# Kernel optimization log

Hardware: AMD Instinct MI355X
Metric: run time of the kernel (lower is better)

## Reference

```python
import jax, jax.numpy as jnp
import numpy as np

B, N, A = 8, 16384, 7
NUM_GROUP = 1024   # npoint / G
GROUP_SIZE = 32    # knn k / M


def setup_inputs() -> dict:
    key = jax.random.key(0)
    xyz = jax.random.uniform(key, (B, N, A), dtype=jnp.float32)
    return {"xyz": xyz}


def _farthest_point_sample(xyz, npoint):
    # xyz: [B, N, A]; distances computed on first 3 dims only.
    b, n, a = xyz.shape
    coords = xyz[:, :, :3]
    batch = jnp.arange(b)
    # Deterministic start index (original uses randint; any start is a valid FPS seed).
    init = (jnp.full((b, n), 1e10, dtype=xyz.dtype), jnp.zeros((b,), dtype=jnp.int32))

    def step(carry, _):
        distance, farthest = carry
        centroid = xyz[batch, farthest]                      # [B, A]
        d = jnp.sum((coords - centroid[:, None, :3]) ** 2, -1)  # [B, N]
        distance = jnp.minimum(distance, d)                  # masked update == min
        new_farthest = jnp.argmax(distance, axis=-1).astype(jnp.int32)
        return (distance, new_farthest), (farthest, centroid)

    _, (idxs, cents) = jax.lax.scan(step, init, None, length=npoint)
    centroids = jnp.swapaxes(idxs, 0, 1)        # [B, npoint]
    centroids_attrs = jnp.swapaxes(cents, 0, 1)  # [B, npoint, A]
    return centroids, centroids_attrs


def _knn(center, xyz, k):
    # Euclidean cdist over ALL A attributes (as in the original torch.cdist call).
    # Squared distance preserves topk ordering.
    c2 = jnp.sum(center ** 2, -1)[:, :, None]    # [B, G, 1]
    x2 = jnp.sum(xyz ** 2, -1)[:, None, :]       # [B, 1, N]
    d2 = c2 + x2 - 2.0 * jnp.einsum('bga,bna->bgn', center, xyz)  # [B, G, N]
    _, idx = jax.lax.top_k(-d2, k)               # smallest-k, ascending distance
    return idx


def reference(xyz):
    center_idx, centroids_attrs = _farthest_point_sample(xyz, NUM_GROUP)
    centroids_coors = centroids_attrs[:, :, :3]
    idx = _knn(centroids_attrs, xyz, GROUP_SIZE)             # [B, G, M]
    b = xyz.shape[0]
    neighborhood = xyz[jnp.arange(b)[:, None, None], idx]    # [B, G, M, A]
    neighborhood = jnp.concatenate(
        [neighborhood[..., :3] - centroids_coors[:, :, None, :],
         neighborhood[..., 3:]], axis=-1)
    return neighborhood, center_idx, centroids_attrs, centroids_coors
```

## Files before the change

### kernel.cpp

```cpp
#include <hip/hip_runtime.h>

#define N_PTS  16384
#define B_SZ   8
#define NGROUP 1024
#define KNN_K  32
#define ATTR   7

#define OFF_NB     0
#define OFF_IDX    (B_SZ * NGROUP * KNN_K * ATTR)
#define OFF_CATTR  (OFF_IDX + B_SZ * NGROUP)
#define OFF_CCOORD (OFF_CATTR + B_SZ * NGROUP * ATTR)

typedef float v2f __attribute__((ext_vector_type(2)));
typedef float f2u __attribute__((ext_vector_type(2), aligned(4)));

template <int CTRL>
__device__ __forceinline__ float fmax_dpp_step(float x) {
    int d = __builtin_amdgcn_update_dpp(__float_as_int(x), __float_as_int(x),
                                        CTRL, 0xf, 0xf, false);
    return fmaxf(x, __int_as_float(d));
}
template <int CTRL>
__device__ __forceinline__ unsigned umin_dpp_step(unsigned x) {
    unsigned d = (unsigned)__builtin_amdgcn_update_dpp((int)x, (int)x,
                                                       CTRL, 0xf, 0xf, false);
    return x < d ? x : d;
}

__device__ __forceinline__ float wave_max_f32(float x) {
    x = fmax_dpp_step<0x111>(x);
    x = fmax_dpp_step<0x112>(x);
    x = fmax_dpp_step<0x114>(x);
    x = fmax_dpp_step<0x118>(x);
    x = fmax_dpp_step<0x142>(x);
    x = fmax_dpp_step<0x143>(x);
    return __int_as_float(__builtin_amdgcn_readlane(__float_as_int(x), 63));
}
__device__ __forceinline__ unsigned wave_min_u32(unsigned x) {
    x = umin_dpp_step<0x111>(x);
    x = umin_dpp_step<0x112>(x);
    x = umin_dpp_step<0x114>(x);
    x = umin_dpp_step<0x118>(x);
    x = umin_dpp_step<0x142>(x);
    x = umin_dpp_step<0x143>(x);
    return (unsigned)__builtin_amdgcn_readlane((int)x, 63);
}

__global__ void prep_kernel(const float* __restrict__ xyz, float* __restrict__ x2,
                            float* __restrict__ xt) {
#pragma clang fp contract(off)
    int i = blockIdx.x * blockDim.x + threadIdx.x;
    if (i >= B_SZ * N_PTS) return;
    const int b = i >> 14;
    const int p = i & (N_PTS - 1);
    const float* q = xyz + (size_t)i * ATTR;
    f2u a01 = *(const f2u*)q;
    f2u a23 = *(const f2u*)(q + 2);
    f2u a45 = *(const f2u*)(q + 4);
    float a6 = q[6];
    float s = a01.x * a01.x;
    s = s + a01.y * a01.y;
    s = s + a23.x * a23.x;
    s = s + a23.y * a23.y;
    s = s + a45.x * a45.x;
    s = s + a45.y * a45.y;
    s = s + a6 * a6;
    x2[i] = s;
    float* T = xt + (size_t)b * ATTR * N_PTS + p;
    T[0 * N_PTS] = a01.x;
    T[1 * N_PTS] = a01.y;
    T[2 * N_PTS] = a23.x;
    T[3 * N_PTS] = a23.y;
    T[4 * N_PTS] = a45.x;
    T[5 * N_PTS] = a45.y;
    T[6 * N_PTS] = a6;
}

#define FOR16(M) M(0) M(1) M(2) M(3) M(4) M(5) M(6) M(7) \
                 M(8) M(9) M(10) M(11) M(12) M(13) M(14) M(15)

#define PT_DECL(J) v2f px##J, py##J, pz##J, pd##J;

#define PT_LOAD(J) { \
    const int p0 = t + ((2 * J) << 9); \
    const float* q0 = X + (size_t)p0 * ATTR; \
    const float* q1 = q0 + (size_t)512 * ATTR; \
    f2u u0 = *(const volatile f2u*)q0; float z0 = ((const volatile float*)q0)[2]; \
    f2u u1 = *(const volatile f2u*)q1; float z1 = ((const volatile float*)q1)[2]; \
    px##J = (v2f){u0.x, u1.x}; \
    py##J = (v2f){u0.y, u1.y}; \
    pz##J = (v2f){z0, z1}; \
    pd##J = (v2f){1e10f, 1e10f}; }

#define PT_STEP(J) { \
    v2f dx = px##J - cx2; \
    v2f dy = py##J - cy2; \
    v2f dz = pz##J - cz2; \
    v2f a  = dx * dx; \
    a = a + dy * dy; \
    a = a + dz * dz; \
    v2f nd; \
    nd.x = fminf(pd##J.x, a.x); \
    nd.y = fminf(pd##J.y, a.y); \
    pd##J = nd; \
    if (nd.x > best) { best = nd.x; bidx = t + ((2 * J) << 9); } \
    if (nd.y > best) { best = nd.y; bidx = t + ((2 * J + 1) << 9); } }

__global__ __launch_bounds__(512)
__attribute__((amdgpu_waves_per_eu(2, 2)))
void fps_kernel(const float* __restrict__ xyz, float* __restrict__ out) {
#pragma clang fp contract(off)
    const int b = blockIdx.x;
    const int t = threadIdx.x;
    const int lane = t & 63;
    const int w = t >> 6;
    const float* X = xyz + (size_t)b * N_PTS * ATTR;

    FOR16(PT_DECL)
    FOR16(PT_LOAD)

    __shared__ unsigned long long sbuf[2][8];
    __shared__ int sel[NGROUP];
    if (t == 0) sel[0] = 0;
    float cx = X[0], cy = X[1], cz = X[2];
    __syncthreads();

    for (int s = 0; s < NGROUP - 1; ++s) {
        const int par = s & 1;
        const v2f cx2 = {cx, cx}, cy2 = {cy, cy}, cz2 = {cz, cz};
        float best = -1.0f;
        int   bidx = 0;
        FOR16(PT_STEP)
        const float wm = wave_max_f32(best);
        const unsigned cand = (best == wm) ? (unsigned)bidx : 0xFFFFFFFFu;
        const unsigned widx = wave_min_u32(cand);
        if (lane == 0) {
            sbuf[par][w] = ((unsigned long long)__float_as_uint(wm) << 32) |
                           (unsigned)(N_PTS - widx);
        }
        __syncthreads();
        unsigned long long bk = sbuf[par][0];
#pragma unroll
        for (int i = 1; i < 8; ++i) {
            const unsigned long long k = sbuf[par][i];
            if (k > bk) bk = k;
        }
        const int win = N_PTS - (int)(unsigned)bk;
        const int sbidx = __builtin_amdgcn_readfirstlane(win);
        if (t == 0) sel[s + 1] = sbidx;
        const float* q = X + (size_t)sbidx * ATTR;
        cx = q[0]; cy = q[1]; cz = q[2];
    }
    __syncthreads();

    for (int g = t; g < NGROUP; g += 512) {
        const int idx = sel[g];
        const float* q = X + (size_t)idx * ATTR;
        float a0 = q[0], a1 = q[1], a2 = q[2], a3 = q[3], a4 = q[4], a5 = q[5], a6 = q[6];
        out[OFF_IDX + b * NGROUP + g] = (float)idx;
        float* ca = out + OFF_CATTR + (size_t)(b * NGROUP + g) * ATTR;
        ca[0] = a0; ca[1] = a1; ca[2] = a2; ca[3] = a3; ca[4] = a4; ca[5] = a5; ca[6] = a6;
        float* cc = out + OFF_CCOORD + (size_t)(b * NGROUP + g) * 3;
        cc[0] = a0; cc[1] = a1; cc[2] = a2;
    }
}

__device__ __forceinline__ void topk_insert(float d2, int p, int lane,
                                            float& ld, int& li, float& kd, int& ki) {
    const bool cand = (d2 < kd) || (d2 == kd && p < ki);
    unsigned long long mask = __ballot(cand);
    while (mask) {
        const int l = __ffsll(mask) - 1;
        mask &= mask - 1;
        const float dc = __shfl(d2, l);
        const int   pc = __shfl(p, l);
        if ((dc < kd) || (dc == kd && pc < ki)) {
            const bool before = (ld < dc) || (ld == dc && li < pc);
            const int pos = (int)__popcll(__ballot(before));
            const float sd = __shfl_up(ld, 1);
            const int   si = __shfl_up(li, 1);
            if (lane == pos)      { ld = dc; li = pc; }
            else if (lane > pos)  { ld = sd; li = si; }
            if (lane >= KNN_K)    { ld = __builtin_inff(); li = 0x7fffffff; }
            kd = __shfl(ld, KNN_K - 1);
            ki = __shfl(li, KNN_K - 1);
        }
    }
}

__global__ __launch_bounds__(256) void knn_kernel(const float* __restrict__ xyz,
                                                  const float* __restrict__ x2,
                                                  const float* __restrict__ xt,
                                                  float* __restrict__ out) {
#pragma clang fp contract(off)
    const int lane = threadIdx.x & 63;
    const int gg = blockIdx.x * 4 + (threadIdx.x >> 6);
    const int b  = gg >> 10;
    const float* X = xyz + (size_t)b * N_PTS * ATTR;

    const float* C = out + OFF_CATTR + (size_t)gg * ATTR;
    const float c0 = C[0], c1 = C[1], c2a = C[2], c3 = C[3], c4 = C[4], c5 = C[5], c6 = C[6];
    float csq = c0 * c0;
    csq = csq + c1 * c1;
    csq = csq + c2a * c2a;
    csq = csq + c3 * c3;
    csq = csq + c4 * c4;
    csq = csq + c5 * c5;
    csq = csq + c6 * c6;

    float ld = __builtin_inff();
    int   li = 0x7fffffff;
    float kd = __builtin_inff();
    int   ki = 0x7fffffff;

    if (xt != nullptr) {
        const float* T0 = xt + (size_t)b * ATTR * N_PTS;
        const float* T1 = T0 + N_PTS;
        const float* T2 = T1 + N_PTS;
        const float* T3 = T2 + N_PTS;
        const float* T4 = T3 + N_PTS;
        const float* T5 = T4 + N_PTS;
        const float* T6 = T5 + N_PTS;
        const float* XB = x2 + (size_t)b * N_PTS;
        for (int p0 = 0; p0 < N_PTS; p0 += 64) {
            const int p = p0 + lane;
            const float q0 = T0[p], q1 = T1[p], q2 = T2[p], q3 = T3[p];
            const float q4 = T4[p], q5 = T5[p], q6 = T6[p];
            float dot = c0 * q0;
            dot = dot + c1 * q1;
            dot = dot + c2a * q2;
            dot = dot + c3 * q3;
            dot = dot + c4 * q4;
            dot = dot + c5 * q5;
            dot = dot + c6 * q6;
            const float xx = XB[p];
            const float d2 = (csq + xx) - 2.0f * dot;
            topk_insert(d2, p, lane, ld, li, kd, ki);
        }
    } else {
        for (int p0 = 0; p0 < N_PTS; p0 += 64) {
            const int p = p0 + lane;
            const float* q = X + (size_t)p * ATTR;
            float dot = c0 * q[0];
            dot = dot + c1 * q[1];
            dot = dot + c2a * q[2];
            dot = dot + c3 * q[3];
            dot = dot + c4 * q[4];
            dot = dot + c5 * q[5];
            dot = dot + c6 * q[6];
            float xx = q[0] * q[0];
            xx = xx + q[1] * q[1];
            xx = xx + q[2] * q[2];
            xx = xx + q[3] * q[3];
            xx = xx + q[4] * q[4];
            xx = xx + q[5] * q[5];
            xx = xx + q[6] * q[6];
            const float d2 = (csq + xx) - 2.0f * dot;
            topk_insert(d2, p, lane, ld, li, kd, ki);
        }
    }

    if (lane < KNN_K) {
        const float* q = X + (size_t)li * ATTR;
        float* o = out + OFF_NB + ((size_t)gg * KNN_K + lane) * ATTR;
        o[0] = q[0] - c0;
        o[1] = q[1] - c1;
        o[2] = q[2] - c2a;
        o[3] = q[3];
        o[4] = q[4];
        o[5] = q[5];
        o[6] = q[6];
    }
}

extern "C" void kernel_launch(void* const* d_in, const int* in_sizes, int n_in,
                              void* d_out, int out_size, void* d_ws, size_t ws_size,
                              hipStream_t stream) {
    const float* xyz = (const float*)d_in[0];
    float* out = (float*)d_out;

    const size_t need = (size_t)(B_SZ * N_PTS) * (1 + ATTR) * sizeof(float);
    const bool use_ws = ws_size >= need;
    float* x2 = use_ws ? (float*)d_ws : nullptr;
    float* xt = use_ws ? ((float*)d_ws + B_SZ * N_PTS) : nullptr;

    if (use_ws) {
        prep_kernel<<<(B_SZ * N_PTS + 255) / 256, 256, 0, stream>>>(xyz, x2, xt);
    }
    fps_kernel<<<B_SZ, 512, 0, stream>>>(xyz, out);
    knn_kernel<<<(B_SZ * NGROUP) / 4, 256, 0, stream>>>(xyz, x2, xt, out);
}
```

Measured before the change: 1.911 ms.

## Move FPS x/y point coordinates from registers to LDS, keep z and distances in VGPRs

The FPS kernel previously held x, y, z and the running min-distance for 32 points per thread in registers. It now stages x and y into shared memory (128 KB of LDS) and rereads them from LDS on every iteration, keeping only z and the distance in registers. An empty asm barrier pins the z values in VGPRs. Point assignment also changes to adjacent point pairs per thread, which gives contiguous loads. The intent is to relieve register pressure and spilling under the 512-thread launch bound, at the cost of 32 LDS reads per thread per FPS step.

```diff
diff --git a/kernel.cpp b/kernel.cpp
--- a/kernel.cpp
+++ b/kernel.cpp
@@ -79,22 +79,23 @@
 #define FOR16(M) M(0) M(1) M(2) M(3) M(4) M(5) M(6) M(7) \
                  M(8) M(9) M(10) M(11) M(12) M(13) M(14) M(15)
 
-#define PT_DECL(J) v2f px##J, py##J, pz##J, pd##J;
-
-#define PT_LOAD(J) { \
-    const int p0 = t + ((2 * J) << 9); \
-    const float* q0 = X + (size_t)p0 * ATTR; \
-    const float* q1 = q0 + (size_t)512 * ATTR; \
-    f2u u0 = *(const volatile f2u*)q0; float z0 = ((const volatile float*)q0)[2]; \
-    f2u u1 = *(const volatile f2u*)q1; float z1 = ((const volatile float*)q1)[2]; \
-    px##J = (v2f){u0.x, u1.x}; \
-    py##J = (v2f){u0.y, u1.y}; \
+#define PZ_DECL(J) v2f pz##J, pd##J;
+
+#define STAGE(J) { \
+    const int q = t + (J << 9); \
+    const float* r0 = X + (size_t)(q << 1) * ATTR; \
+    f2u u0 = *(const f2u*)r0;          float z0 = r0[2]; \
+    f2u u1 = *(const f2u*)(r0 + ATTR); float z1 = r0[2 + ATTR]; \
+    lx[q] = (v2f){u0.x, u1.x}; \
+    ly[q] = (v2f){u0.y, u1.y}; \
     pz##J = (v2f){z0, z1}; \
     pd##J = (v2f){1e10f, 1e10f}; }
 
 #define PT_STEP(J) { \
-    v2f dx = px##J - cx2; \
-    v2f dy = py##J - cy2; \
+    const v2f pxv = lx[t + (J << 9)]; \
+    const v2f pyv = ly[t + (J << 9)]; \
+    v2f dx = pxv - cx2; \
+    v2f dy = pyv - cy2; \
     v2f dz = pz##J - cz2; \
     v2f a  = dx * dx; \
     a = a + dy * dy; \
@@ -103,8 +104,8 @@
     nd.x = fminf(pd##J.x, a.x); \
     nd.y = fminf(pd##J.y, a.y); \
     pd##J = nd; \
-    if (nd.x > best) { best = nd.x; bidx = t + ((2 * J) << 9); } \
-    if (nd.y > best) { best = nd.y; bidx = t + ((2 * J + 1) << 9); } }
+    if (nd.x > best) { best = nd.x; bidx = (t << 1) + (J << 10); } \
+    if (nd.y > best) { best = nd.y; bidx = (t << 1) + (J << 10) + 1; } }
 
 __global__ __launch_bounds__(512)
 __attribute__((amdgpu_waves_per_eu(2, 2)))
@@ -116,17 +117,24 @@
     const int w = t >> 6;
     const float* X = xyz + (size_t)b * N_PTS * ATTR;
 
-    FOR16(PT_DECL)
-    FOR16(PT_LOAD)
-
+    __shared__ v2f lx[N_PTS / 2];
+    __shared__ v2f ly[N_PTS / 2];
+    __shared__ int sel[NGROUP];
     __shared__ unsigned long long sbuf[2][8];
-    __shared__ int sel[NGROUP];
+
+    FOR16(PZ_DECL)
+    FOR16(STAGE)
+
     if (t == 0) sel[0] = 0;
     float cx = X[0], cy = X[1], cz = X[2];
     __syncthreads();
 
     for (int s = 0; s < NGROUP - 1; ++s) {
         const int par = s & 1;
+        asm volatile("" : "+v"(pz0), "+v"(pz1), "+v"(pz2), "+v"(pz3),
+                          "+v"(pz4), "+v"(pz5), "+v"(pz6), "+v"(pz7),
+                          "+v"(pz8), "+v"(pz9), "+v"(pz10), "+v"(pz11),
+                          "+v"(pz12), "+v"(pz13), "+v"(pz14), "+v"(pz15));
         const v2f cx2 = {cx, cx}, cy2 = {cy, cy}, cz2 = {cz, cz};
         float best = -1.0f;
         int   bidx = 0;
```

New measurement: 2.070 ms. 1.08x slower.

## Double FPS block size to 1024 threads with 16 points per thread

Applied to the files above, without the earlier changes.

The farthest-point-sampling kernel now runs 1024 threads per batch instead of 512. Each thread holds 16 points in registers instead of 32, and the point assignment changes to adjacent pairs so loads are contiguous. The block-level reduction now merges 16 wave results, and empty asm statements pin the point coordinates in VGPRs. This halves the serial per-step work per thread, at the cost of more waves joining each barrier and a larger cross-wave reduction on every one of the 1023 iterations.

```diff
diff --git a/kernel.cpp b/kernel.cpp
--- a/kernel.cpp
+++ b/kernel.cpp
@@ -76,17 +76,15 @@
     T[6 * N_PTS] = a6;
 }
 
-#define FOR16(M) M(0) M(1) M(2) M(3) M(4) M(5) M(6) M(7) \
-                 M(8) M(9) M(10) M(11) M(12) M(13) M(14) M(15)
+#define FOR8(M) M(0) M(1) M(2) M(3) M(4) M(5) M(6) M(7)
 
 #define PT_DECL(J) v2f px##J, py##J, pz##J, pd##J;
 
 #define PT_LOAD(J) { \
-    const int p0 = t + ((2 * J) << 9); \
-    const float* q0 = X + (size_t)p0 * ATTR; \
-    const float* q1 = q0 + (size_t)512 * ATTR; \
-    f2u u0 = *(const volatile f2u*)q0; float z0 = ((const volatile float*)q0)[2]; \
-    f2u u1 = *(const volatile f2u*)q1; float z1 = ((const volatile float*)q1)[2]; \
+    const int q = t + (J << 10); \
+    const float* r0 = X + (size_t)(q << 1) * ATTR; \
+    f2u u0 = *(const f2u*)r0;          float z0 = r0[2]; \
+    f2u u1 = *(const f2u*)(r0 + ATTR); float z1 = r0[2 + ATTR]; \
     px##J = (v2f){u0.x, u1.x}; \
     py##J = (v2f){u0.y, u1.y}; \
     pz##J = (v2f){z0, z1}; \
@@ -103,11 +101,11 @@
     nd.x = fminf(pd##J.x, a.x); \
     nd.y = fminf(pd##J.y, a.y); \
     pd##J = nd; \
-    if (nd.x > best) { best = nd.x; bidx = t + ((2 * J) << 9); } \
-    if (nd.y > best) { best = nd.y; bidx = t + ((2 * J + 1) << 9); } }
-
-__global__ __launch_bounds__(512)
-__attribute__((amdgpu_waves_per_eu(2, 2)))
+    if (nd.x > best) { best = nd.x; bidx = (t << 1) + (J << 11); } \
+    if (nd.y > best) { best = nd.y; bidx = (t << 1) + (J << 11) + 1; } }
+
+__global__ __launch_bounds__(1024)
+__attribute__((amdgpu_waves_per_eu(4, 4)))
 void fps_kernel(const float* __restrict__ xyz, float* __restrict__ out) {
 #pragma clang fp contract(off)
     const int b = blockIdx.x;
@@ -116,10 +114,10 @@
     const int w = t >> 6;
     const float* X = xyz + (size_t)b * N_PTS * ATTR;
 
-    FOR16(PT_DECL)
-    FOR16(PT_LOAD)
-
-    __shared__ unsigned long long sbuf[2][8];
+    FOR8(PT_DECL)
+    FOR8(PT_LOAD)
+
+    __shared__ unsigned long long sbuf[2][16];
     __shared__ int sel[NGROUP];
     if (t == 0) sel[0] = 0;
     float cx = X[0], cy = X[1], cz = X[2];
@@ -127,10 +125,16 @@
 
     for (int s = 0; s < NGROUP - 1; ++s) {
         const int par = s & 1;
+        asm volatile("" : "+v"(px0), "+v"(px1), "+v"(px2), "+v"(px3),
+                          "+v"(px4), "+v"(px5), "+v"(px6), "+v"(px7));
+        asm volatile("" : "+v"(py0), "+v"(py1), "+v"(py2), "+v"(py3),
+                          "+v"(py4), "+v"(py5), "+v"(py6), "+v"(py7));
+        asm volatile("" : "+v"(pz0), "+v"(pz1), "+v"(pz2), "+v"(pz3),
+                          "+v"(pz4), "+v"(pz5), "+v"(pz6), "+v"(pz7));
         const v2f cx2 = {cx, cx}, cy2 = {cy, cy}, cz2 = {cz, cz};
         float best = -1.0f;
         int   bidx = 0;
-        FOR16(PT_STEP)
+        FOR8(PT_STEP)
         const float wm = wave_max_f32(best);
         const unsigned cand = (best == wm) ? (unsigned)bidx : 0xFFFFFFFFu;
         const unsigned widx = wave_min_u32(cand);
@@ -141,7 +145,7 @@
         __syncthreads();
         unsigned long long bk = sbuf[par][0];
 #pragma unroll
-        for (int i = 1; i < 8; ++i) {
+        for (int i = 1; i < 16; ++i) {
             const unsigned long long k = sbuf[par][i];
             if (k > bk) bk = k;
         }
@@ -153,7 +157,8 @@
     }
     __syncthreads();
 
-    for (int g = t; g < NGROUP; g += 512) {
+    {
+        const int g = t;
         const int idx = sel[g];
         const float* q = X + (size_t)idx * ATTR;
         float a0 = q[0], a1 = q[1], a2 = q[2], a3 = q[3], a4 = q[4], a5 = q[5], a6 = q[6];
@@ -287,6 +292,6 @@
     if (use_ws) {
         prep_kernel<<<(B_SZ * N_PTS + 255) / 256, 256, 0, stream>>>(xyz, x2, xt);
     }
-    fps_kernel<<<B_SZ, 512, 0, stream>>>(xyz, out);
+    fps_kernel<<<B_SZ, 1024, 0, stream>>>(xyz, out);
     knn_kernel<<<(B_SZ * NGROUP) / 4, 256, 0, stream>>>(xyz, x2, xt, out);
 }
```

Result: slower. 2.056 ms (+7.6%).

## Use LDS atomicMax for FPS reduction and split KNN scan across two waves

Applied to the files above, without the earlier changes.

In the FPS kernel, the per-wave argmax keys now go into a rotating triple-buffered shared slot through atomicMax. This replaces the 8-entry buffer that every thread scanned after the barrier. In the KNN kernel, each group's point scan is split between two waves, each covering half the points, and the two top-k lists are merged through shared memory, doubling the number of blocks. The aim is to shorten the serial per-step FPS reduction and to raise KNN parallelism, at the cost of an extra merge pass and a block-wide barrier.

```diff
diff --git a/kernel.cpp b/kernel.cpp
--- a/kernel.cpp
+++ b/kernel.cpp
@@ -113,20 +113,18 @@
     const int b = blockIdx.x;
     const int t = threadIdx.x;
     const int lane = t & 63;
-    const int w = t >> 6;
     const float* X = xyz + (size_t)b * N_PTS * ATTR;
 
     FOR16(PT_DECL)
     FOR16(PT_LOAD)
 
-    __shared__ unsigned long long sbuf[2][8];
+    __shared__ unsigned long long slot[3];
     __shared__ int sel[NGROUP];
-    if (t == 0) sel[0] = 0;
+    if (t == 0) { slot[0] = 0ull; sel[0] = 0; }
     float cx = X[0], cy = X[1], cz = X[2];
     __syncthreads();
 
     for (int s = 0; s < NGROUP - 1; ++s) {
-        const int par = s & 1;
         const v2f cx2 = {cx, cx}, cy2 = {cy, cy}, cz2 = {cz, cz};
         float best = -1.0f;
         int   bidx = 0;
@@ -135,16 +133,14 @@
         const unsigned cand = (best == wm) ? (unsigned)bidx : 0xFFFFFFFFu;
         const unsigned widx = wave_min_u32(cand);
         if (lane == 0) {
-            sbuf[par][w] = ((unsigned long long)__float_as_uint(wm) << 32) |
-                           (unsigned)(N_PTS - widx);
-        }
+            const unsigned long long key =
+                ((unsigned long long)__float_as_uint(wm) << 32) |
+                (unsigned)(N_PTS - widx);
+            atomicMax(&slot[s % 3], key);
+        }
+        if (t == 0) slot[(s + 1) % 3] = 0ull;
         __syncthreads();
-        unsigned long long bk = sbuf[par][0];
-#pragma unroll
-        for (int i = 1; i < 8; ++i) {
-            const unsigned long long k = sbuf[par][i];
-            if (k > bk) bk = k;
-        }
+        const unsigned long long bk = slot[s % 3];
         const int win = N_PTS - (int)(unsigned)bk;
         const int sbidx = __builtin_amdgcn_readfirstlane(win);
         if (t == 0) sel[s + 1] = sbidx;
@@ -194,7 +190,10 @@
                                                   float* __restrict__ out) {
 #pragma clang fp contract(off)
     const int lane = threadIdx.x & 63;
-    const int gg = blockIdx.x * 4 + (threadIdx.x >> 6);
+    const int w    = threadIdx.x >> 6;
+    const int gib  = w >> 1;
+    const int half = w & 1;
+    const int gg = blockIdx.x * 2 + gib;
     const int b  = gg >> 10;
     const float* X = xyz + (size_t)b * N_PTS * ATTR;
 
@@ -213,6 +212,9 @@
     float kd = __builtin_inff();
     int   ki = 0x7fffffff;
 
+    const int pbeg = half * (N_PTS / 2);
+    const int pend = pbeg + (N_PTS / 2);
+
     if (xt != nullptr) {
         const float* T0 = xt + (size_t)b * ATTR * N_PTS;
         const float* T1 = T0 + N_PTS;
@@ -222,7 +224,7 @@
         const float* T5 = T4 + N_PTS;
         const float* T6 = T5 + N_PTS;
         const float* XB = x2 + (size_t)b * N_PTS;
-        for (int p0 = 0; p0 < N_PTS; p0 += 64) {
+        for (int p0 = pbeg; p0 < pend; p0 += 64) {
             const int p = p0 + lane;
             const float q0 = T0[p], q1 = T1[p], q2 = T2[p], q3 = T3[p];
             const float q4 = T4[p], q5 = T5[p], q6 = T6[p];
@@ -238,7 +240,7 @@
             topk_insert(d2, p, lane, ld, li, kd, ki);
         }
     } else {
-        for (int p0 = 0; p0 < N_PTS; p0 += 64) {
+        for (int p0 = pbeg; p0 < pend; p0 += 64) {
             const int p = p0 + lane;
             const float* q = X + (size_t)p * ATTR;
             float dot = c0 * q[0];
@@ -260,16 +262,30 @@
         }
     }
 
+    __shared__ float smd[2][2][KNN_K];
+    __shared__ int   smi[2][2][KNN_K];
     if (lane < KNN_K) {
-        const float* q = X + (size_t)li * ATTR;
-        float* o = out + OFF_NB + ((size_t)gg * KNN_K + lane) * ATTR;
-        o[0] = q[0] - c0;
-        o[1] = q[1] - c1;
-        o[2] = q[2] - c2a;
-        o[3] = q[3];
-        o[4] = q[4];
-        o[5] = q[5];
-        o[6] = q[6];
+        smd[gib][half][lane] = ld;
+        smi[gib][half][lane] = li;
+    }
+    __syncthreads();
+
+    if (half == 0) {
+        const float dc2 = (lane < KNN_K) ? smd[gib][1][lane] : __builtin_inff();
+        const int   pc2 = (lane < KNN_K) ? smi[gib][1][lane] : 0x7fffffff;
+        topk_insert(dc2, pc2, lane, ld, li, kd, ki);
+
+        if (lane < KNN_K) {
+            const float* q = X + (size_t)li * ATTR;
+            float* o = out + OFF_NB + ((size_t)gg * KNN_K + lane) * ATTR;
+            o[0] = q[0] - c0;
+            o[1] = q[1] - c1;
+            o[2] = q[2] - c2a;
+            o[3] = q[3];
+            o[4] = q[4];
+            o[5] = q[5];
+            o[6] = q[6];
+        }
     }
 }
 
@@ -288,5 +304,5 @@
         prep_kernel<<<(B_SZ * N_PTS + 255) / 256, 256, 0, stream>>>(xyz, x2, xt);
     }
     fps_kernel<<<B_SZ, 512, 0, stream>>>(xyz, out);
-    knn_kernel<<<(B_SZ * NGROUP) / 4, 256, 0, stream>>>(xyz, x2, xt, out);
-}
+    knn_kernel<<<(B_SZ * NGROUP) / 2, 256, 0, stream>>>(xyz, x2, xt, out);
+}
```

Result: no change. 1.948 ms (+1.9%).
